# Kernel tuning notes

Hardware: AMD Instinct MI355X
Metric: run time of the kernel (lower is better)

Reference implementation:

```python
import jax, jax.numpy as jnp
import numpy as np

N = 16384       # input points
D_IN = 64       # feature dim
D_OUT = 128     # output dim
STRIDE = 4      # downsampling stride -> M = N // STRIDE sampled points
NSAMPLE = 16    # hard-coded in __init__
BN_EPS = 1e-5


def setup_inputs() -> dict:
    key = jax.random.key(0)
    k1, k2, k3 = jax.random.split(key, 3)
    p = jax.random.normal(k1, (N, 3), jnp.float32)
    x = jax.random.normal(k2, (N, D_IN), jnp.float32)
    o = jnp.array([N], jnp.int32)  # single-cloud offsets
    # mlp params: Linear(d_in+3, d_out) + BatchNorm1d(d_out)
    W = jax.random.normal(k3, (D_IN + 3, D_OUT), jnp.float32) * 0.05
    b = jnp.zeros((D_OUT,), jnp.float32)
    gamma = jnp.ones((D_OUT,), jnp.float32)
    beta = jnp.zeros((D_OUT,), jnp.float32)
    return {"p": p, "x": x, "o": o, "W": W, "b": b, "gamma": gamma, "beta": beta}


def fps(p, m):
    """Furthest point sampling: returns m indices into p [N,3]. Sequential by nature."""
    n = p.shape[0]
    dists = jnp.full((n,), jnp.inf, p.dtype)
    idxs = jnp.zeros((m,), jnp.int32)  # start from point 0 (pointops convention)

    def body(i, carry):
        idxs, dists = carry
        last = p[idxs[i - 1]]                      # [3]
        d = jnp.sum((p - last) ** 2, axis=1)       # [N]
        dists = jnp.minimum(dists, d)
        return idxs.at[i].set(jnp.argmax(dists).astype(jnp.int32)), dists

    idxs, _ = jax.lax.fori_loop(1, m, body, (idxs, dists))
    return idxs


def reference(p, x, o, W, b, gamma, beta):
    m = p.shape[0] // STRIDE  # static
    # --- furthest point sampling (non-differentiable index op, as in pointops) ---
    s_idx = fps(jax.lax.stop_gradient(p), m)
    n_p = p[s_idx]                                             # [M,3]
    # --- query-and-group: kNN of each sampled point over all N points ---
    d2 = (jnp.sum(n_p ** 2, axis=1)[:, None]
          + jnp.sum(p ** 2, axis=1)[None, :]
          - 2.0 * n_p @ p.T)                                   # [M,N]
    _, nn_idx = jax.lax.top_k(-d2, NSAMPLE)                    # [M,K]
    pj = p[nn_idx] - n_p[:, None, :]                           # [M,K,3] relative coords
    xj = x[nn_idx]                                             # [M,K,D_IN]
    # normalize relative coords by max neighbor norm per sampled point
    nrm = jnp.linalg.norm(pj, axis=-1, keepdims=True)          # [M,K,1]
    pj = pj / (jnp.max(nrm, axis=1, keepdims=True) + 1e-8)
    feat = jnp.concatenate([pj, xj], axis=-1).max(axis=1)      # [M, 3+D_IN] max-pool
    # --- MLP: Linear + BatchNorm1d (training stats) + ReLU ---
    h = feat @ W + b                                           # [M, D_OUT]
    mean = jnp.mean(h, axis=0)
    var = jnp.var(h, axis=0)
    h = (h - mean) / jnp.sqrt(var + BN_EPS) * gamma + beta
    x_out = jax.nn.relu(h)
    n_o = jnp.array([m], jnp.int32)
    return (n_p, x_out, n_o)
```

## Files before the change

kernel.cpp:

```cpp
#include <hip/hip_runtime.h>

#define N_PTS 16384
#define M_PTS 4096
#define D_INF 64
#define D_OUTF 128
#define KNN 16
#define DF 67

__global__ __launch_bounds__(256) void sp_kernel(const float* __restrict__ p,
                                                 float* __restrict__ spn) {
  int j = blockIdx.x * 256 + threadIdx.x;
  float a = p[3 * j], b = p[3 * j + 1], c = p[3 * j + 2];
  spn[j] = __fadd_rn(__fadd_rn(__fmul_rn(a, a), __fmul_rn(b, b)), __fmul_rn(c, c));
}

#define FPS_T 512
#define FPS_PPT 32

__global__ __launch_bounds__(FPS_T, 2) void fps_kernel(const float* __restrict__ p,
                                                       int* __restrict__ sidx,
                                                       float* __restrict__ np_out) {
  const int t = threadIdx.x;
  float px[FPS_PPT], py[FPS_PPT], pz[FPS_PPT], dd[FPS_PPT];
#pragma unroll
  for (int k = 0; k < FPS_PPT; ++k) {
    int j = t + (k << 9);
    px[k] = p[3 * j]; py[k] = p[3 * j + 1]; pz[k] = p[3 * j + 2];
    dd[k] = INFINITY;
  }
  __shared__ float s_v[2][FPS_T / 64];
  __shared__ int   s_i[2][FPS_T / 64];
  if (t == 0) {
    sidx[0] = 0;
    np_out[0] = p[0]; np_out[1] = p[1]; np_out[2] = p[2];
  }
  float lx = p[0], ly = p[1], lz = p[2];
  for (int i = 1; i < M_PTS; ++i) {
    float tmax = -INFINITY;
#pragma unroll
    for (int k = 0; k < FPS_PPT; ++k) {
      float dx = __fsub_rn(px[k], lx);
      float dy = __fsub_rn(py[k], ly);
      float dz = __fsub_rn(pz[k], lz);
      float d = __fadd_rn(__fadd_rn(__fmul_rn(dx, dx), __fmul_rn(dy, dy)),
                          __fmul_rn(dz, dz));
      float nd = fminf(dd[k], d);
      dd[k] = nd;
      tmax = fmaxf(tmax, nd);
    }
    int bk = 0;
#pragma unroll
    for (int k = FPS_PPT - 1; k >= 0; --k) {
      if (dd[k] == tmax) bk = k;
    }
    int ri = t + (bk << 9);
    float rv = tmax;
#pragma unroll
    for (int off = 32; off >= 1; off >>= 1) {
      float ov = __shfl_xor(rv, off);
      int   oi = __shfl_xor(ri, off);
      bool tk = (ov > rv) || (ov == rv && oi < ri);
      rv = tk ? ov : rv;
      ri = tk ? oi : ri;
    }
    const int par = i & 1;
    if ((t & 63) == 0) { s_v[par][t >> 6] = rv; s_i[par][t >> 6] = ri; }
    __syncthreads();
    float gv = s_v[par][0];
    int   gi = s_i[par][0];
#pragma unroll
    for (int w = 1; w < FPS_T / 64; ++w) {
      float ov = s_v[par][w];
      int   oi = s_i[par][w];
      bool tk = (ov > gv) || (ov == gv && oi < gi);
      gv = tk ? ov : gv;
      gi = tk ? oi : gi;
    }
    lx = p[3 * gi]; ly = p[3 * gi + 1]; lz = p[3 * gi + 2];
    if (t == 0) {
      sidx[i] = gi;
      np_out[3 * i] = lx; np_out[3 * i + 1] = ly; np_out[3 * i + 2] = lz;
    }
  }
}

__global__ __launch_bounds__(256) void knn_feat_kernel(const float* __restrict__ p,
                                                       const float* __restrict__ x,
                                                       const float* __restrict__ spn,
                                                       const int* __restrict__ sidx,
                                                       float* __restrict__ feat) {
  __shared__ float cd[4][256];
  __shared__ int ci[4][256];
  __shared__ int cnt[4];
  __shared__ int s_nn[4][KNN];
  const int w = threadIdx.x >> 6;
  const int lane = threadIdx.x & 63;
  const int q = (blockIdx.x << 2) + w;
  const int qi = sidx[q];
  const float qx = p[3 * qi], qy = p[3 * qi + 1], qz = p[3 * qi + 2];
  const float sn = spn[qi];
  if (lane == 0) cnt[w] = 0;
  float lmin = INFINITY;
  for (int it = 0; it < N_PTS / 64; ++it) {
    int j = lane + (it << 6);
    float dot = __fmaf_rn(qz, p[3 * j + 2],
                 __fmaf_rn(qy, p[3 * j + 1], __fmul_rn(qx, p[3 * j])));
    float d2 = __fsub_rn(__fadd_rn(sn, spn[j]), __fmul_rn(2.0f, dot));
    lmin = fminf(lmin, d2);
  }
  float mv = lmin;
  float tau = INFINITY;
#pragma unroll
  for (int r = 0; r < KNN; ++r) {
    float rmin = mv;
#pragma unroll
    for (int off = 32; off >= 1; off >>= 1) rmin = fminf(rmin, __shfl_xor(rmin, off));
    tau = rmin;
    unsigned long long msk = __ballot(mv == rmin);
    if (lane == (int)(__ffsll(msk) - 1)) mv = INFINITY;
  }
  __syncthreads();
  for (int it = 0; it < N_PTS / 64; ++it) {
    int j = lane + (it << 6);
    float dot = __fmaf_rn(qz, p[3 * j + 2],
                 __fmaf_rn(qy, p[3 * j + 1], __fmul_rn(qx, p[3 * j])));
    float d2 = __fsub_rn(__fadd_rn(sn, spn[j]), __fmul_rn(2.0f, dot));
    if (d2 <= tau) {
      int pos = atomicAdd(&cnt[w], 1);
      if (pos < 256) { cd[w][pos] = d2; ci[w][pos] = j; }
    }
  }
  __syncthreads();
  int C = min(cnt[w], 256);
  float vv[4]; int ii[4];
#pragma unroll
  for (int s = 0; s < 4; ++s) {
    int pos = lane + (s << 6);
    bool ok = pos < C;
    vv[s] = ok ? cd[w][pos] : INFINITY;
    ii[s] = ok ? ci[w][pos] : 0x7FFFFFFF;
  }
#pragma unroll
  for (int r = 0; r < KNN; ++r) {
    float bv = vv[0]; int bi = ii[0]; int bs = 0;
#pragma unroll
    for (int s = 1; s < 4; ++s) {
      bool tk = (vv[s] < bv) || (vv[s] == bv && ii[s] < bi);
      bv = tk ? vv[s] : bv; bi = tk ? ii[s] : bi; bs = tk ? s : bs;
    }
    float rv = bv; int ri = bi;
#pragma unroll
    for (int off = 32; off >= 1; off >>= 1) {
      float ov = __shfl_xor(rv, off); int oi = __shfl_xor(ri, off);
      bool tk = (ov < rv) || (ov == rv && oi < ri);
      rv = tk ? ov : rv; ri = tk ? oi : ri;
    }
    if (bi == ri) {
#pragma unroll
      for (int s = 0; s < 4; ++s) if (s == bs) vv[s] = INFINITY;
    }
    if (lane == 0) s_nn[w][r] = ri;
  }
  __syncthreads();
  float ax = -INFINITY, ay = -INFINITY, az = -INFINITY, nr = -INFINITY;
  if (lane < KNN) {
    int jn = s_nn[w][lane];
    ax = __fsub_rn(p[3 * jn], qx);
    ay = __fsub_rn(p[3 * jn + 1], qy);
    az = __fsub_rn(p[3 * jn + 2], qz);
    nr = sqrtf(__fadd_rn(__fadd_rn(__fmul_rn(ax, ax), __fmul_rn(ay, ay)),
                         __fmul_rn(az, az)));
  }
  float mnr = nr, mx = ax, my = ay, mz = az;
#pragma unroll
  for (int off = 32; off >= 1; off >>= 1) {
    mnr = fmaxf(mnr, __shfl_xor(mnr, off));
    mx = fmaxf(mx, __shfl_xor(mx, off));
    my = fmaxf(my, __shfl_xor(my, off));
    mz = fmaxf(mz, __shfl_xor(mz, off));
  }
  if (lane == 0) {
    float sden = __fadd_rn(mnr, 1e-8f);
    feat[q * DF + 0] = mx / sden;
    feat[q * DF + 1] = my / sden;
    feat[q * DF + 2] = mz / sden;
  }
  float fm = -INFINITY;
#pragma unroll
  for (int k = 0; k < KNN; ++k) {
    int jn = s_nn[w][k];
    fm = fmaxf(fm, x[(jn << 6) + lane]);
  }
  feat[q * DF + 3 + lane] = fm;
}

__global__ __launch_bounds__(128) void mlp_kernel(const float* __restrict__ feat,
                                                  const float* __restrict__ W,
                                                  const float* __restrict__ b,
                                                  float* __restrict__ h) {
  int mrow = blockIdx.x;
  int o = threadIdx.x;
  const float* fr = feat + mrow * DF;
  float acc = b[o];
#pragma unroll
  for (int k = 0; k < DF; ++k) acc = __fmaf_rn(fr[k], W[k * D_OUTF + o], acc);
  h[mrow * D_OUTF + o] = acc;
}

__global__ __launch_bounds__(256) void stats_kernel(const float* __restrict__ h,
                                                    const float* __restrict__ gamma,
                                                    const float* __restrict__ beta,
                                                    float* __restrict__ scsh) {
  int o = blockIdx.x;
  int t = threadIdx.x;
  float s = 0.f, s2 = 0.f;
  for (int mrow = t; mrow < M_PTS; mrow += 256) {
    float v = h[mrow * D_OUTF + o];
    s += v;
    s2 = __fmaf_rn(v, v, s2);
  }
#pragma unroll
  for (int off = 32; off >= 1; off >>= 1) {
    s += __shfl_xor(s, off);
    s2 += __shfl_xor(s2, off);
  }
  __shared__ float as1[4], as2[4];
  if ((t & 63) == 0) { as1[t >> 6] = s; as2[t >> 6] = s2; }
  __syncthreads();
  if (t == 0) {
    float ts = ((as1[0] + as1[1]) + as1[2]) + as1[3];
    float ts2 = ((as2[0] + as2[1]) + as2[2]) + as2[3];
    float mean = ts / (float)M_PTS;
    float var = ts2 / (float)M_PTS - mean * mean;
    var = fmaxf(var, 0.f);
    float sc = gamma[o] / sqrtf(var + 1e-5f);
    scsh[o] = sc;
    scsh[D_OUTF + o] = beta[o] - mean * sc;
  }
}

__global__ __launch_bounds__(256) void bn_kernel(const float* __restrict__ h,
                                                 const float* __restrict__ scsh,
                                                 float* __restrict__ out) {
  int idx = blockIdx.x * 256 + threadIdx.x;
  int o = idx & (D_OUTF - 1);
  float v = __fmaf_rn(h[idx], scsh[o], scsh[D_OUTF + o]);
  out[M_PTS * 3 + idx] = fmaxf(v, 0.f);
  if (idx == 0) out[M_PTS * 3 + M_PTS * D_OUTF] = 4096.0f;
}

extern "C" void kernel_launch(void* const* d_in, const int* in_sizes, int n_in,
                              void* d_out, int out_size, void* d_ws, size_t ws_size,
                              hipStream_t stream) {
  const float* p     = (const float*)d_in[0];
  const float* x     = (const float*)d_in[1];
  const float* W     = (const float*)d_in[3];
  const float* b     = (const float*)d_in[4];
  const float* gamma = (const float*)d_in[5];
  const float* beta  = (const float*)d_in[6];
  float* out = (float*)d_out;

  float* wsf  = (float*)d_ws;
  int*   sidx = (int*)d_ws;
  float* spn  = wsf + 4096;
  float* feat = spn + N_PTS;
  float* h    = feat + M_PTS * DF;
  float* scsh = h + M_PTS * D_OUTF;

  sp_kernel<<<N_PTS / 256, 256, 0, stream>>>(p, spn);
  fps_kernel<<<1, FPS_T, 0, stream>>>(p, sidx, out);
  knn_feat_kernel<<<M_PTS / 4, 256, 0, stream>>>(p, x, spn, sidx, feat);
  mlp_kernel<<<M_PTS, D_OUTF, 0, stream>>>(feat, W, b, h);
  stats_kernel<<<D_OUTF, 256, 0, stream>>>(h, gamma, beta, scsh);
  bn_kernel<<<(M_PTS * D_OUTF) / 256, 256, 0, stream>>>(h, scsh, out);
}
```

Baseline: 8.623 ms.

## Bucket points into spatial grid cells and prune FPS updates by cell bounds

```diff
diff --git a/kernel.cpp b/kernel.cpp
--- a/kernel.cpp
+++ b/kernel.cpp
@@ -15,70 +15,222 @@
 }
 
 #define FPS_T 512
-#define FPS_PPT 32
-
-__global__ __launch_bounds__(FPS_T, 2) void fps_kernel(const float* __restrict__ p,
-                                                       int* __restrict__ sidx,
-                                                       float* __restrict__ np_out) {
+#define NW (FPS_T / 64)
+#define GRD 8
+#define CELLS 512
+
+__global__ __launch_bounds__(FPS_T) void fps_kernel(const float* __restrict__ p,
+                                                    int* __restrict__ sidx,
+                                                    float* __restrict__ np_out,
+                                                    float4* __restrict__ ppk) {
   const int t = threadIdx.x;
-  float px[FPS_PPT], py[FPS_PPT], pz[FPS_PPT], dd[FPS_PPT];
-#pragma unroll
-  for (int k = 0; k < FPS_PPT; ++k) {
+  const int lane = t & 63;
+  const int w = t >> 6;
+
+  __shared__ float s_dd[N_PTS];
+  __shared__ float s_blo[3][CELLS];
+  __shared__ float s_bhi[3][CELLS];
+  __shared__ float s_bmax[CELLS];
+  __shared__ int   s_bidx[CELLS];
+  __shared__ int   s_bpos[CELLS];
+  __shared__ int   s_start[CELLS];
+  __shared__ int   s_cnt[CELLS];
+  __shared__ int   s_aff[CELLS];
+  __shared__ int   s_ofs[CELLS];
+  __shared__ float s_mm[NW][8];
+  __shared__ int   s_wsum[NW];
+  __shared__ float4 s_red[NW];
+  __shared__ int   s_naff;
+
+  float mlx = INFINITY, mly = INFINITY, mlz = INFINITY;
+  float mhx = -INFINITY, mhy = -INFINITY, mhz = -INFINITY;
+  for (int k = 0; k < N_PTS / FPS_T; ++k) {
     int j = t + (k << 9);
-    px[k] = p[3 * j]; py[k] = p[3 * j + 1]; pz[k] = p[3 * j + 2];
-    dd[k] = INFINITY;
-  }
-  __shared__ float s_v[2][FPS_T / 64];
-  __shared__ int   s_i[2][FPS_T / 64];
+    float a = p[3 * j], b = p[3 * j + 1], c = p[3 * j + 2];
+    mlx = fminf(mlx, a); mly = fminf(mly, b); mlz = fminf(mlz, c);
+    mhx = fmaxf(mhx, a); mhy = fmaxf(mhy, b); mhz = fmaxf(mhz, c);
+  }
+#pragma unroll
+  for (int off = 32; off >= 1; off >>= 1) {
+    mlx = fminf(mlx, __shfl_xor(mlx, off));
+    mly = fminf(mly, __shfl_xor(mly, off));
+    mlz = fminf(mlz, __shfl_xor(mlz, off));
+    mhx = fmaxf(mhx, __shfl_xor(mhx, off));
+    mhy = fmaxf(mhy, __shfl_xor(mhy, off));
+    mhz = fmaxf(mhz, __shfl_xor(mhz, off));
+  }
+  if (lane == 0) {
+    s_mm[w][0] = mlx; s_mm[w][1] = mly; s_mm[w][2] = mlz;
+    s_mm[w][3] = mhx; s_mm[w][4] = mhy; s_mm[w][5] = mhz;
+  }
+  __syncthreads();
+  float glox = s_mm[0][0], gloy = s_mm[0][1], gloz = s_mm[0][2];
+  float ghix = s_mm[0][3], ghiy = s_mm[0][4], ghiz = s_mm[0][5];
+#pragma unroll
+  for (int w2 = 1; w2 < NW; ++w2) {
+    glox = fminf(glox, s_mm[w2][0]); gloy = fminf(gloy, s_mm[w2][1]);
+    gloz = fminf(gloz, s_mm[w2][2]);
+    ghix = fmaxf(ghix, s_mm[w2][3]); ghiy = fmaxf(ghiy, s_mm[w2][4]);
+    ghiz = fmaxf(ghiz, s_mm[w2][5]);
+  }
+  const float invx = (float)GRD / (ghix - glox);
+  const float invy = (float)GRD / (ghiy - gloy);
+  const float invz = (float)GRD / (ghiz - gloz);
+
+#define CELL_OF(A, B, C, OUT)                                            \
+  do {                                                                   \
+    int cx_ = (int)(((A) - glox) * invx);                                \
+    int cy_ = (int)(((B) - gloy) * invy);                                \
+    int cz_ = (int)(((C) - gloz) * invz);                                \
+    cx_ = max(0, min(GRD - 1, cx_));                                     \
+    cy_ = max(0, min(GRD - 1, cy_));                                     \
+    cz_ = max(0, min(GRD - 1, cz_));                                     \
+    OUT = (cx_ * GRD + cy_) * GRD + cz_;                                 \
+  } while (0)
+
+  s_cnt[t] = 0;
+  __syncthreads();
+  for (int k = 0; k < N_PTS / FPS_T; ++k) {
+    int j = t + (k << 9);
+    int cell; CELL_OF(p[3 * j], p[3 * j + 1], p[3 * j + 2], cell);
+    atomicAdd(&s_cnt[cell], 1);
+  }
+  __syncthreads();
+  {
+    int c0 = s_cnt[t];
+    int inc = c0;
+#pragma unroll
+    for (int off = 1; off <= 32; off <<= 1) {
+      int o = __shfl_up(inc, off);
+      if (lane >= off) inc += o;
+    }
+    if (lane == 63) s_wsum[w] = inc;
+    __syncthreads();
+    int woff = 0;
+    for (int w2 = 0; w2 < w; ++w2) woff += s_wsum[w2];
+    int ex = woff + inc - c0;
+    s_start[t] = ex;
+    s_ofs[t] = ex;
+  }
+  __syncthreads();
+  for (int k = 0; k < N_PTS / FPS_T; ++k) {
+    int j = t + (k << 9);
+    float a = p[3 * j], b = p[3 * j + 1], c = p[3 * j + 2];
+    int cell; CELL_OF(a, b, c, cell);
+    int pos = atomicAdd(&s_ofs[cell], 1);
+    ppk[pos] = make_float4(a, b, c, __int_as_float(j));
+    s_dd[pos] = INFINITY;
+  }
+  __syncthreads();
+  for (int bkt = w; bkt < CELLS; bkt += NW) {
+    int s = s_start[bkt], e = s + s_cnt[bkt];
+    float blx = INFINITY, bly = INFINITY, blz = INFINITY;
+    float bhx = -INFINITY, bhy = -INFINITY, bhz = -INFINITY;
+    for (int j = s + lane; j < e; j += 64) {
+      float4 f = ppk[j];
+      blx = fminf(blx, f.x); bly = fminf(bly, f.y); blz = fminf(blz, f.z);
+      bhx = fmaxf(bhx, f.x); bhy = fmaxf(bhy, f.y); bhz = fmaxf(bhz, f.z);
+    }
+#pragma unroll
+    for (int off = 32; off >= 1; off >>= 1) {
+      blx = fminf(blx, __shfl_xor(blx, off));
+      bly = fminf(bly, __shfl_xor(bly, off));
+      blz = fminf(blz, __shfl_xor(blz, off));
+      bhx = fmaxf(bhx, __shfl_xor(bhx, off));
+      bhy = fmaxf(bhy, __shfl_xor(bhy, off));
+      bhz = fmaxf(bhz, __shfl_xor(bhz, off));
+    }
+    if (lane == 0) {
+      s_blo[0][bkt] = blx; s_blo[1][bkt] = bly; s_blo[2][bkt] = blz;
+      s_bhi[0][bkt] = bhx; s_bhi[1][bkt] = bhy; s_bhi[2][bkt] = bhz;
+      s_bmax[bkt] = (s_cnt[bkt] > 0) ? INFINITY : -INFINITY;
+      s_bidx[bkt] = 0x7FFFFFFF;
+      s_bpos[bkt] = 0;
+    }
+  }
   if (t == 0) {
+    s_naff = 0;
     sidx[0] = 0;
     np_out[0] = p[0]; np_out[1] = p[1]; np_out[2] = p[2];
   }
   float lx = p[0], ly = p[1], lz = p[2];
+  __syncthreads();
+
   for (int i = 1; i < M_PTS; ++i) {
-    float tmax = -INFINITY;
-#pragma unroll
-    for (int k = 0; k < FPS_PPT; ++k) {
-      float dx = __fsub_rn(px[k], lx);
-      float dy = __fsub_rn(py[k], ly);
-      float dz = __fsub_rn(pz[k], lz);
-      float d = __fadd_rn(__fadd_rn(__fmul_rn(dx, dx), __fmul_rn(dy, dy)),
-                          __fmul_rn(dz, dz));
-      float nd = fminf(dd[k], d);
-      dd[k] = nd;
-      tmax = fmaxf(tmax, nd);
-    }
-    int bk = 0;
-#pragma unroll
-    for (int k = FPS_PPT - 1; k >= 0; --k) {
-      if (dd[k] == tmax) bk = k;
-    }
-    int ri = t + (bk << 9);
-    float rv = tmax;
+    {
+      const int bb = t;
+      float ax = __fsub_rn(s_blo[0][bb], lx);
+      float bx = __fsub_rn(lx, s_bhi[0][bb]);
+      float dxb = fmaxf(fmaxf(ax, bx), 0.0f);
+      float ay = __fsub_rn(s_blo[1][bb], ly);
+      float by = __fsub_rn(ly, s_bhi[1][bb]);
+      float dyb = fmaxf(fmaxf(ay, by), 0.0f);
+      float az = __fsub_rn(s_blo[2][bb], lz);
+      float bz = __fsub_rn(lz, s_bhi[2][bb]);
+      float dzb = fmaxf(fmaxf(az, bz), 0.0f);
+      float dsq = __fadd_rn(__fadd_rn(__fmul_rn(dxb, dxb), __fmul_rn(dyb, dyb)),
+                            __fmul_rn(dzb, dzb));
+      if (dsq < s_bmax[bb]) {
+        int pos = atomicAdd(&s_naff, 1);
+        s_aff[pos] = bb;
+      }
+    }
+    __syncthreads();
+    const int naff = s_naff;
+    for (int a = w; a < naff; a += NW) {
+      const int bkt = s_aff[a];
+      const int s = s_start[bkt], e = s + s_cnt[bkt];
+      float v = -INFINITY; int oi = 0x7FFFFFFF, pj = 0;
+      for (int j = s + lane; j < e; j += 64) {
+        float4 f = ppk[j];
+        float dx = __fsub_rn(f.x, lx);
+        float dy = __fsub_rn(f.y, ly);
+        float dz = __fsub_rn(f.z, lz);
+        float d = __fadd_rn(__fadd_rn(__fmul_rn(dx, dx), __fmul_rn(dy, dy)),
+                            __fmul_rn(dz, dz));
+        float nd = fminf(s_dd[j], d);
+        s_dd[j] = nd;
+        int o = __float_as_int(f.w);
+        bool tk = (nd > v) || (nd == v && o < oi);
+        v = tk ? nd : v; oi = tk ? o : oi; pj = tk ? j : pj;
+      }
+#pragma unroll
+      for (int off = 32; off >= 1; off >>= 1) {
+        float ov = __shfl_xor(v, off);
+        int ooi = __shfl_xor(oi, off);
+        int opj = __shfl_xor(pj, off);
+        bool tk = (ov > v) || (ov == v && ooi < oi);
+        v = tk ? ov : v; oi = tk ? ooi : oi; pj = tk ? opj : pj;
+      }
+      if (lane == 0) { s_bmax[bkt] = v; s_bidx[bkt] = oi; s_bpos[bkt] = pj; }
+    }
+    __syncthreads();
+    float v = s_bmax[t]; int oi = s_bidx[t], pj = s_bpos[t];
 #pragma unroll
     for (int off = 32; off >= 1; off >>= 1) {
-      float ov = __shfl_xor(rv, off);
-      int   oi = __shfl_xor(ri, off);
-      bool tk = (ov > rv) || (ov == rv && oi < ri);
-      rv = tk ? ov : rv;
-      ri = tk ? oi : ri;
-    }
-    const int par = i & 1;
-    if ((t & 63) == 0) { s_v[par][t >> 6] = rv; s_i[par][t >> 6] = ri; }
+      float ov = __shfl_xor(v, off);
+      int ooi = __shfl_xor(oi, off);
+      int opj = __shfl_xor(pj, off);
+      bool tk = (ov > v) || (ov == v && ooi < oi);
+      v = tk ? ov : v; oi = tk ? ooi : oi; pj = tk ? opj : pj;
+    }
+    if (lane == 0) s_red[w] = make_float4(v, __int_as_float(oi), __int_as_float(pj), 0.f);
+    if (t == 0) s_naff = 0;
     __syncthreads();
-    float gv = s_v[par][0];
-    int   gi = s_i[par][0];
-#pragma unroll
-    for (int w = 1; w < FPS_T / 64; ++w) {
-      float ov = s_v[par][w];
-      int   oi = s_i[par][w];
-      bool tk = (ov > gv) || (ov == gv && oi < gi);
-      gv = tk ? ov : gv;
-      gi = tk ? oi : gi;
-    }
-    lx = p[3 * gi]; ly = p[3 * gi + 1]; lz = p[3 * gi + 2];
+    float4 e0 = s_red[0];
+    float gv = e0.x; int goi = __float_as_int(e0.y), gpj = __float_as_int(e0.z);
+#pragma unroll
+    for (int w2 = 1; w2 < NW; ++w2) {
+      float4 e = s_red[w2];
+      float ov = e.x; int ooi = __float_as_int(e.y);
+      bool tk = (ov > gv) || (ov == gv && ooi < goi);
+      gv = tk ? ov : gv; goi = tk ? ooi : goi;
+      gpj = tk ? __float_as_int(e.z) : gpj;
+    }
+    float4 wf = ppk[gpj];
+    lx = wf.x; ly = wf.y; lz = wf.z;
     if (t == 0) {
-      sidx[i] = gi;
+      sidx[i] = goi;
       np_out[3 * i] = lx; np_out[3 * i + 1] = ly; np_out[3 * i + 2] = lz;
     }
   }
@@ -267,8 +419,10 @@
   float* h    = feat + M_PTS * DF;
   float* scsh = h + M_PTS * D_OUTF;
 
+  float4* ppk = (float4*)h;
+
   sp_kernel<<<N_PTS / 256, 256, 0, stream>>>(p, spn);
-  fps_kernel<<<1, FPS_T, 0, stream>>>(p, sidx, out);
+  fps_kernel<<<1, FPS_T, 0, stream>>>(p, sidx, out, ppk);
   knn_feat_kernel<<<M_PTS / 4, 256, 0, stream>>>(p, x, spn, sidx, feat);
   mlp_kernel<<<M_PTS, D_OUTF, 0, stream>>>(feat, W, b, h);
   stats_kernel<<<D_OUTF, 256, 0, stream>>>(h, gamma, beta, scsh);
```

After: 11.92 ms. 38.2% more time.
